# Performance work log

Hardware: AMD Instinct MI355X
Metric: run time of the kernel (lower is better)

## Reference

```python
import jax, jax.numpy as jnp
import numpy as np

N_TOPICS = 256
BATCH = 131072


def setup_inputs() -> dict:
    key = jax.random.key(0)
    k = jax.random.split(key, 6)
    n, b = N_TOPICS, BATCH
    s = 1.0 / np.sqrt(n)  # matches torch RNNCell uniform(-1/sqrt(h), 1/sqrt(h)) scale
    return {
        "z": jax.random.normal(k[0], (b, n), jnp.float32),
        "h0": jax.random.uniform(k[1], (1, n), jnp.float32),
        "W_ih": jax.random.uniform(k[2], (n, n), jnp.float32, -s, s),
        "W_hh": jax.random.uniform(k[3], (n, n), jnp.float32, -s, s),
        "b_ih": jax.random.uniform(k[4], (n,), jnp.float32, -s, s),
        "b_hh": jax.random.uniform(k[5], (n,), jnp.float32, -s, s),
    }


def _stick_breaking(x):
    # torch.distributions.StickBreakingTransform._call
    D = x.shape[-1]
    offset = jnp.arange(D, 0, -1, dtype=x.dtype)          # [D, D-1, ..., 1]
    zc = jax.nn.sigmoid(x - jnp.log(offset))
    fi = jnp.finfo(x.dtype)
    zc = jnp.clip(zc, fi.tiny, 1.0 - fi.eps)              # _clipped_sigmoid
    z_cumprod = jnp.cumprod(1.0 - zc, axis=-1)
    ones = jnp.ones(x.shape[:-1] + (1,), x.dtype)
    return jnp.concatenate([zc, ones], -1) * jnp.concatenate([ones, z_cumprod], -1)


def reference(z, h0, W_ih, W_hh, b_ih, b_hh):
    n = W_ih.shape[0]
    D = n - 1
    b = b_ih + b_hh
    # step 0: rnncell(h0) with zero hidden state -> tanh(h0 @ W_ih.T + b_ih + b_hh)
    h1 = jnp.tanh(h0 @ W_ih.T + b)                        # (1, n)
    # steps i>0: rnncell(h, h) = tanh(h @ (W_ih + W_hh).T + b_ih + b_hh)
    Wc = (W_ih + W_hh).T

    def step(h, _):
        hn = jnp.tanh(h @ Wc + b)
        return hn, hn

    _, hs = jax.lax.scan(step, h1, None, length=D - 1)    # (D-1, 1, n)
    H = jnp.concatenate([h1[None], hs], axis=0)[:, 0, :]  # (D, n)
    eta = jax.nn.sigmoid(H @ z.T).T                       # (batch, D)
    return _stick_breaking(eta)                           # (batch, n)
```

## Files before the change

### kernel.cpp

```cpp
#include <hip/hip_runtime.h>

#define NTOP 256

typedef __attribute__((ext_vector_type(8))) short bf16x8;
typedef __attribute__((ext_vector_type(4))) float f32x4;

__device__ inline unsigned int packbf(float x) {
  unsigned int u = __float_as_uint(x);
  unsigned int r = (u + 0x7fffu + ((u >> 16) & 1u)) & 0xffff0000u;
  float res = x - __uint_as_float(r);
  unsigned int u2 = __float_as_uint(res);
  unsigned int r2 = u2 + 0x7fffu + ((u2 >> 16) & 1u);
  return r | (r2 >> 16);
}

__device__ inline float tanh_fast(float x) {
  float e = __expf(2.f * x);
  return 1.f - 2.f / (e + 1.f);
}

__global__ __launch_bounds__(1024) void rsbc_recur(
    const float* __restrict__ Wih, const float* __restrict__ Whh,
    const float* __restrict__ bih, const float* __restrict__ bhh,
    const float* __restrict__ h0, unsigned int* __restrict__ Hpack) {
  __shared__ float hA[4][68], hB[4][68];
  const int tid = threadIdx.x;
  const int j = tid >> 2, qt = tid & 3, k0 = qt * 64;
  const float bj = bih[j] + bhh[j];

  float4 w[16];
  const float4* wp = reinterpret_cast<const float4*>(Wih + j * NTOP + k0);
#pragma unroll
  for (int q = 0; q < 16; ++q) w[q] = wp[q];

  if (tid < NTOP) hA[tid >> 6][tid & 63] = h0[tid];
  __syncthreads();

  {
    const float* hq = hA[qt];
    float a0 = 0.f, a1 = 0.f, a2 = 0.f, a3 = 0.f;
#pragma unroll
    for (int q = 0; q < 16; ++q) {
      float4 hv = *reinterpret_cast<const float4*>(hq + 4 * q);
      a0 += hv.x * w[q].x; a1 += hv.y * w[q].y;
      a2 += hv.z * w[q].z; a3 += hv.w * w[q].w;
    }
    float s = (a0 + a1) + (a2 + a3);
    s += __shfl_xor(s, 1);
    s += __shfl_xor(s, 2);
    if (qt == 0) {
      float v = tanh_fast(s + bj);
      hB[j >> 6][j & 63] = v;
      Hpack[j] = packbf(v);
    }
  }
  const float4* wq = reinterpret_cast<const float4*>(Whh + j * NTOP + k0);
#pragma unroll
  for (int q = 0; q < 16; ++q) {
    float4 t = wq[q];
    w[q].x += t.x; w[q].y += t.y; w[q].z += t.z; w[q].w += t.w;
  }
  __syncthreads();

  for (int s = 1; s < 255; ++s) {
    const float(*hr)[68] = (s & 1) ? hB : hA;
    float(*hw)[68] = (s & 1) ? hA : hB;
    const float* hq = hr[qt];
    float a0 = 0.f, a1 = 0.f, a2 = 0.f, a3 = 0.f;
#pragma unroll
    for (int q = 0; q < 16; ++q) {
      float4 hv = *reinterpret_cast<const float4*>(hq + 4 * q);
      a0 += hv.x * w[q].x; a1 += hv.y * w[q].y;
      a2 += hv.z * w[q].z; a3 += hv.w * w[q].w;
    }
    float sv = (a0 + a1) + (a2 + a3);
    sv += __shfl_xor(sv, 1);
    sv += __shfl_xor(sv, 2);
    if (qt == 0) {
      float v = tanh_fast(sv + bj);
      hw[j >> 6][j & 63] = v;
      Hpack[s * NTOP + j] = packbf(v);
    }
    __syncthreads();
  }
}

__global__ __launch_bounds__(512, 2) void rsbc_gemm_sb(
    const float* __restrict__ z, const unsigned int* __restrict__ Hpack,
    float* __restrict__ out) {
  constexpr int AS = 72;
  constexpr int BS = 72;
  constexpr int ES = 260;
  __shared__ __align__(16) char smem[135168];
  __shared__ float logtab[256];
  ushort* Ahi = reinterpret_cast<ushort*>(smem);
  ushort* Alo = Ahi + 128 * AS;
  ushort* Bhi = Alo + 128 * AS;
  ushort* Blo = Bhi + 256 * BS;
  float* eta = reinterpret_cast<float*>(smem);
  float* segT = eta + 128 * ES;

  const int tid = threadIdx.x;
  const size_t row0 = (size_t)blockIdx.x * 128;
  const int wid = tid >> 6, lane = tid & 63;
  const int wr = wid >> 2, wc = wid & 3;
  const int l15 = lane & 15, l4 = lane >> 4;

  if (tid < 255) logtab[tid] = logf((float)(255 - tid));

  f32x4 acc[4][4];
#pragma unroll
  for (int mt = 0; mt < 4; ++mt)
#pragma unroll
    for (int nt = 0; nt < 4; ++nt) acc[mt][nt] = (f32x4){0.f, 0.f, 0.f, 0.f};

  for (int kc = 0; kc < 4; ++kc) {
    const int kb = kc * 64;
    float4 zreg[4];
#pragma unroll
    for (int it = 0; it < 4; ++it) {
      int idx = tid + 512 * it;
      int r = idx >> 4, q = idx & 15;
      zreg[it] = *reinterpret_cast<const float4*>(
          z + (row0 + r) * NTOP + kb + 4 * q);
    }
    uint4 hreg[8];
#pragma unroll
    for (int it = 0; it < 8; ++it) {
      int idx = tid + 512 * it;
      int r = idx >> 4, q = idx & 15;
      hreg[it] = (r < 255)
                     ? *reinterpret_cast<const uint4*>(
                           Hpack + r * NTOP + kb + 4 * q)
                     : make_uint4(0u, 0u, 0u, 0u);
    }
    __syncthreads();
#pragma unroll
    for (int it = 0; it < 4; ++it) {
      int idx = tid + 512 * it;
      int r = idx >> 4, q = idx & 15;
      float4 v = zreg[it];
      unsigned int p0 = packbf(v.x), p1 = packbf(v.y),
                   p2 = packbf(v.z), p3 = packbf(v.w);
      *reinterpret_cast<ushort4*>(&Ahi[r * AS + 4 * q]) = make_ushort4(
          (ushort)(p0 >> 16), (ushort)(p1 >> 16),
          (ushort)(p2 >> 16), (ushort)(p3 >> 16));
      *reinterpret_cast<ushort4*>(&Alo[r * AS + 4 * q]) = make_ushort4(
          (ushort)(p0 & 0xffff), (ushort)(p1 & 0xffff),
          (ushort)(p2 & 0xffff), (ushort)(p3 & 0xffff));
    }
#pragma unroll
    for (int it = 0; it < 8; ++it) {
      int idx = tid + 512 * it;
      int r = idx >> 4, q = idx & 15;
      uint4 hv = hreg[it];
      *reinterpret_cast<ushort4*>(&Bhi[r * BS + 4 * q]) = make_ushort4(
          (ushort)(hv.x >> 16), (ushort)(hv.y >> 16),
          (ushort)(hv.z >> 16), (ushort)(hv.w >> 16));
      *reinterpret_cast<ushort4*>(&Blo[r * BS + 4 * q]) = make_ushort4(
          (ushort)(hv.x & 0xffff), (ushort)(hv.y & 0xffff),
          (ushort)(hv.z & 0xffff), (ushort)(hv.w & 0xffff));
    }
    __syncthreads();
#pragma unroll
    for (int ks = 0; ks < 2; ++ks) {
      const int ko = ks * 32 + l4 * 8;
      bf16x8 afh[4], afl[4], bfh[4], bfl[4];
#pragma unroll
      for (int mt = 0; mt < 4; ++mt) {
        int r = 64 * wr + 16 * mt + l15;
        afh[mt] = *reinterpret_cast<const bf16x8*>(&Ahi[r * AS + ko]);
        afl[mt] = *reinterpret_cast<const bf16x8*>(&Alo[r * AS + ko]);
      }
#pragma unroll
      for (int nt = 0; nt < 4; ++nt) {
        int n = 64 * wc + 16 * nt + l15;
        bfh[nt] = *reinterpret_cast<const bf16x8*>(&Bhi[n * BS + ko]);
        bfl[nt] = *reinterpret_cast<const bf16x8*>(&Blo[n * BS + ko]);
      }
#pragma unroll
      for (int mt = 0; mt < 4; ++mt)
#pragma unroll
        for (int nt = 0; nt < 4; ++nt) {
          acc[mt][nt] = __builtin_amdgcn_mfma_f32_16x16x32_bf16(
              afh[mt], bfh[nt], acc[mt][nt], 0, 0, 0);
          acc[mt][nt] = __builtin_amdgcn_mfma_f32_16x16x32_bf16(
              afh[mt], bfl[nt], acc[mt][nt], 0, 0, 0);
          acc[mt][nt] = __builtin_amdgcn_mfma_f32_16x16x32_bf16(
              afl[mt], bfh[nt], acc[mt][nt], 0, 0, 0);
        }
    }
  }
  __syncthreads();

#pragma unroll
  for (int mt = 0; mt < 4; ++mt) {
    int rbase = 64 * wr + 16 * mt + 4 * l4;
#pragma unroll
    for (int nt = 0; nt < 4; ++nt) {
      int c = 64 * wc + 16 * nt + l15;
#pragma unroll
      for (int i = 0; i < 4; ++i) {
        float x = acc[mt][nt][i];
        eta[(rbase + i) * ES + c] = 1.f / (1.f + __expf(-x));
      }
    }
  }
  __syncthreads();

  const int r = tid >> 2, qk = tid & 3;
  const int kbeg = 64 * qk, kend = (qk == 3) ? 255 : 64 * qk + 64;
  float* er = &eta[r * ES];
  {
    float cp = 1.f;
#pragma unroll 4
    for (int k = kbeg; k < kend; ++k) {
      float x = er[k] - logtab[k];
      float zc = 1.f / (1.f + __expf(-x));
      zc = fminf(fmaxf(zc, 1.1754943508222875e-38f), 0.99999988079071045f);
      er[k] = zc * cp;
      cp *= 1.f - zc;
    }
    segT[r * 4 + qk] = cp;
  }
  __syncthreads();
  {
    float p = 1.f;
    if (qk > 0) p *= segT[r * 4 + 0];
    if (qk > 1) p *= segT[r * 4 + 1];
    if (qk > 2) p *= segT[r * 4 + 2];
    if (qk > 0) {
#pragma unroll 4
      for (int k = kbeg; k < kend; ++k) er[k] *= p;
    }
    if (qk == 3) er[255] = p * segT[r * 4 + 3];
  }
  __syncthreads();

#pragma unroll
  for (int it = 0; it < 16; ++it) {
    int idx = tid + 512 * it;
    int rr = idx >> 6, cq = idx & 63;
    float4 vv = *reinterpret_cast<const float4*>(&eta[rr * ES + 4 * cq]);
    *reinterpret_cast<float4*>(&out[(row0 + rr) * NTOP + 4 * cq]) = vv;
  }
}

extern "C" void kernel_launch(void* const* d_in, const int* in_sizes, int n_in,
                              void* d_out, int out_size, void* d_ws, size_t ws_size,
                              hipStream_t stream) {
  const float* z   = (const float*)d_in[0];
  const float* h0  = (const float*)d_in[1];
  const float* Wih = (const float*)d_in[2];
  const float* Whh = (const float*)d_in[3];
  const float* bih = (const float*)d_in[4];
  const float* bhh = (const float*)d_in[5];
  float* out = (float*)d_out;
  unsigned int* Hpack = (unsigned int*)d_ws;

  rsbc_recur<<<1, 1024, 0, stream>>>(Wih, Whh, bih, bhh, h0, Hpack);
  const int nrows = out_size / NTOP;
  const int blocks = nrows / 128;
  rsbc_gemm_sb<<<blocks, 512, 0, stream>>>(z, Hpack, out);
}
```

Measured before the change: 335.1 us.

## Rework recurrence partitioning and fuse stick-breaking scan into GEMM epilogue registers

The recurrence kernel now splits each dot product across waves, combining partial sums through shared memory with DPP reductions. The GEMM kernel moves to a smaller K-chunk with XOR-swizzled shared tiles, cutting LDS use to allow more blocks per CU. The stick-breaking cumulative product is now done as a log-space prefix scan in registers on the accumulators (DPP scan16 plus a cross-wave row total). This removes the eta shared-memory round trip and the serial per-row loop, and output is stored straight from registers. The log-space product (exp of summed softplus) can differ numerically from the direct cumprod, the explicit clip is gone, and the output stores are 4-byte strided rather than float4.

```diff
diff --git a/kernel.cpp b/kernel.cpp
--- a/kernel.cpp
+++ b/kernel.cpp
@@ -19,86 +19,94 @@
   return 1.f - 2.f / (e + 1.f);
 }
 
-__global__ __launch_bounds__(1024) void rsbc_recur(
+template <int CTRL>
+__device__ inline float dpp_f(float v) {
+  return __int_as_float(__builtin_amdgcn_update_dpp(
+      0, __float_as_int(v), CTRL, 0xf, 0xf, true));
+}
+
+__device__ inline float scan16(float v) {
+  float s = v;
+  s += dpp_f<0x111>(s);
+  s += dpp_f<0x112>(s);
+  s += dpp_f<0x114>(s);
+  s += dpp_f<0x118>(s);
+  return s;
+}
+
+__global__ __launch_bounds__(1024, 4) void rsbc_recur(
     const float* __restrict__ Wih, const float* __restrict__ Whh,
     const float* __restrict__ bih, const float* __restrict__ bhh,
     const float* __restrict__ h0, unsigned int* __restrict__ Hpack) {
-  __shared__ float hA[4][68], hB[4][68];
+  __shared__ __align__(16) float hsh[NTOP];
+  __shared__ __align__(16) float pw[16 * 260];
   const int tid = threadIdx.x;
-  const int j = tid >> 2, qt = tid & 3, k0 = qt * 64;
-  const float bj = bih[j] + bhh[j];
-
-  float4 w[16];
-  const float4* wp = reinterpret_cast<const float4*>(Wih + j * NTOP + k0);
-#pragma unroll
-  for (int q = 0; q < 16; ++q) w[q] = wp[q];
-
-  if (tid < NTOP) hA[tid >> 6][tid & 63] = h0[tid];
+  const int w = tid >> 6, l = tid & 63;
+  const int jr = tid >> 2, p4 = tid & 3;
+  const float bj = bih[jr] + bhh[jr];
+
+  float4 L[16];
+#pragma unroll
+  for (int c = 0; c < 4; ++c)
+#pragma unroll
+    for (int g = 0; g < 4; ++g)
+      L[4 * c + g] = *reinterpret_cast<const float4*>(
+          Wih + (4 * l + c) * NTOP + 16 * w + 4 * g);
+
+  if (tid < NTOP) hsh[tid] = h0[tid];
   __syncthreads();
 
-  {
-    const float* hq = hA[qt];
-    float a0 = 0.f, a1 = 0.f, a2 = 0.f, a3 = 0.f;
-#pragma unroll
-    for (int q = 0; q < 16; ++q) {
-      float4 hv = *reinterpret_cast<const float4*>(hq + 4 * q);
-      a0 += hv.x * w[q].x; a1 += hv.y * w[q].y;
-      a2 += hv.z * w[q].z; a3 += hv.w * w[q].w;
-    }
-    float s = (a0 + a1) + (a2 + a3);
-    s += __shfl_xor(s, 1);
-    s += __shfl_xor(s, 2);
-    if (qt == 0) {
-      float v = tanh_fast(s + bj);
-      hB[j >> 6][j & 63] = v;
-      Hpack[j] = packbf(v);
+#pragma unroll 1
+  for (int s = 0; s < 255; ++s) {
+    float4 hv[4];
+#pragma unroll
+    for (int g = 0; g < 4; ++g)
+      hv[g] = *reinterpret_cast<const float4*>(hsh + 16 * w + 4 * g);
+    float a[4] = {0.f, 0.f, 0.f, 0.f};
+#pragma unroll
+    for (int c = 0; c < 4; ++c)
+#pragma unroll
+      for (int g = 0; g < 4; ++g) {
+        a[c] += hv[g].x * L[4 * c + g].x;
+        a[c] += hv[g].y * L[4 * c + g].y;
+        a[c] += hv[g].z * L[4 * c + g].z;
+        a[c] += hv[g].w * L[4 * c + g].w;
+      }
+    *reinterpret_cast<float4*>(&pw[w * 260 + 4 * l]) =
+        make_float4(a[0], a[1], a[2], a[3]);
+    __syncthreads();
+    float v = pw[(4 * p4 + 0) * 260 + jr] + pw[(4 * p4 + 1) * 260 + jr] +
+              pw[(4 * p4 + 2) * 260 + jr] + pw[(4 * p4 + 3) * 260 + jr];
+    v += dpp_f<0xB1>(v);
+    v += dpp_f<0x4E>(v);
+    if (p4 == 0) {
+      float hn = tanh_fast(v + bj);
+      hsh[jr] = hn;
+      Hpack[s * NTOP + jr] = packbf(hn);
+    }
+    __syncthreads();
+    if (s == 0) {
+#pragma unroll
+      for (int c = 0; c < 4; ++c)
+#pragma unroll
+        for (int g = 0; g < 4; ++g) {
+          float4 t = *reinterpret_cast<const float4*>(
+              Whh + (4 * l + c) * NTOP + 16 * w + 4 * g);
+          L[4 * c + g].x += t.x; L[4 * c + g].y += t.y;
+          L[4 * c + g].z += t.z; L[4 * c + g].w += t.w;
+        }
     }
   }
-  const float4* wq = reinterpret_cast<const float4*>(Whh + j * NTOP + k0);
-#pragma unroll
-  for (int q = 0; q < 16; ++q) {
-    float4 t = wq[q];
-    w[q].x += t.x; w[q].y += t.y; w[q].z += t.z; w[q].w += t.w;
-  }
-  __syncthreads();
-
-  for (int s = 1; s < 255; ++s) {
-    const float(*hr)[68] = (s & 1) ? hB : hA;
-    float(*hw)[68] = (s & 1) ? hA : hB;
-    const float* hq = hr[qt];
-    float a0 = 0.f, a1 = 0.f, a2 = 0.f, a3 = 0.f;
-#pragma unroll
-    for (int q = 0; q < 16; ++q) {
-      float4 hv = *reinterpret_cast<const float4*>(hq + 4 * q);
-      a0 += hv.x * w[q].x; a1 += hv.y * w[q].y;
-      a2 += hv.z * w[q].z; a3 += hv.w * w[q].w;
-    }
-    float sv = (a0 + a1) + (a2 + a3);
-    sv += __shfl_xor(sv, 1);
-    sv += __shfl_xor(sv, 2);
-    if (qt == 0) {
-      float v = tanh_fast(sv + bj);
-      hw[j >> 6][j & 63] = v;
-      Hpack[s * NTOP + j] = packbf(v);
-    }
-    __syncthreads();
-  }
-}
-
-__global__ __launch_bounds__(512, 2) void rsbc_gemm_sb(
+}
+
+__global__ __launch_bounds__(512, 4) void rsbc_gemm_sb(
     const float* __restrict__ z, const unsigned int* __restrict__ Hpack,
     float* __restrict__ out) {
-  constexpr int AS = 72;
-  constexpr int BS = 72;
-  constexpr int ES = 260;
-  __shared__ __align__(16) char smem[135168];
-  __shared__ float logtab[256];
-  ushort* Ahi = reinterpret_cast<ushort*>(smem);
-  ushort* Alo = Ahi + 128 * AS;
-  ushort* Bhi = Alo + 128 * AS;
-  ushort* Blo = Bhi + 256 * BS;
-  float* eta = reinterpret_cast<float*>(smem);
-  float* segT = eta + 128 * ES;
+  __shared__ __align__(16) char smem[49152];
+  __shared__ float logtab[NTOP];
+  __shared__ float rowT[128 * 5];
+  char* Ab = smem;
+  char* Bb = smem + 16384;
 
   const int tid = threadIdx.x;
   const size_t row0 = (size_t)blockIdx.x * 128;
@@ -106,7 +114,7 @@
   const int wr = wid >> 2, wc = wid & 3;
   const int l15 = lane & 15, l4 = lane >> 4;
 
-  if (tid < 255) logtab[tid] = logf((float)(255 - tid));
+  if (tid < NTOP) logtab[tid] = (tid < 255) ? __logf((float)(255 - tid)) : 0.f;
 
   f32x4 acc[4][4];
 #pragma unroll
@@ -114,136 +122,130 @@
 #pragma unroll
     for (int nt = 0; nt < 4; ++nt) acc[mt][nt] = (f32x4){0.f, 0.f, 0.f, 0.f};
 
-  for (int kc = 0; kc < 4; ++kc) {
-    const int kb = kc * 64;
-    float4 zreg[4];
-#pragma unroll
-    for (int it = 0; it < 4; ++it) {
-      int idx = tid + 512 * it;
-      int r = idx >> 4, q = idx & 15;
+  for (int kc = 0; kc < 8; ++kc) {
+    const int kb = kc * 32;
+    float4 zreg[2];
+#pragma unroll
+    for (int it = 0; it < 2; ++it) {
+      int idx = tid + 512 * it;
+      int r = idx >> 3, q = idx & 7;
       zreg[it] = *reinterpret_cast<const float4*>(
           z + (row0 + r) * NTOP + kb + 4 * q);
     }
-    uint4 hreg[8];
-#pragma unroll
-    for (int it = 0; it < 8; ++it) {
-      int idx = tid + 512 * it;
-      int r = idx >> 4, q = idx & 15;
-      hreg[it] = (r < 255)
-                     ? *reinterpret_cast<const uint4*>(
-                           Hpack + r * NTOP + kb + 4 * q)
-                     : make_uint4(0u, 0u, 0u, 0u);
-    }
-    __syncthreads();
+    uint4 hreg[4];
 #pragma unroll
     for (int it = 0; it < 4; ++it) {
       int idx = tid + 512 * it;
-      int r = idx >> 4, q = idx & 15;
+      int r = idx >> 3, q = idx & 7;
+      hreg[it] = (r < 255) ? *reinterpret_cast<const uint4*>(
+                                 Hpack + r * NTOP + kb + 4 * q)
+                           : make_uint4(0u, 0u, 0u, 0u);
+    }
+    __syncthreads();
+#pragma unroll
+    for (int it = 0; it < 2; ++it) {
+      int idx = tid + 512 * it;
+      int r = idx >> 3, q = idx & 7;
+      int sw = (r & 7) << 4;
       float4 v = zreg[it];
       unsigned int p0 = packbf(v.x), p1 = packbf(v.y),
                    p2 = packbf(v.z), p3 = packbf(v.w);
-      *reinterpret_cast<ushort4*>(&Ahi[r * AS + 4 * q]) = make_ushort4(
-          (ushort)(p0 >> 16), (ushort)(p1 >> 16),
-          (ushort)(p2 >> 16), (ushort)(p3 >> 16));
-      *reinterpret_cast<ushort4*>(&Alo[r * AS + 4 * q]) = make_ushort4(
-          (ushort)(p0 & 0xffff), (ushort)(p1 & 0xffff),
-          (ushort)(p2 & 0xffff), (ushort)(p3 & 0xffff));
-    }
-#pragma unroll
-    for (int it = 0; it < 8; ++it) {
-      int idx = tid + 512 * it;
-      int r = idx >> 4, q = idx & 15;
-      uint4 hv = hreg[it];
-      *reinterpret_cast<ushort4*>(&Bhi[r * BS + 4 * q]) = make_ushort4(
-          (ushort)(hv.x >> 16), (ushort)(hv.y >> 16),
-          (ushort)(hv.z >> 16), (ushort)(hv.w >> 16));
-      *reinterpret_cast<ushort4*>(&Blo[r * BS + 4 * q]) = make_ushort4(
-          (ushort)(hv.x & 0xffff), (ushort)(hv.y & 0xffff),
-          (ushort)(hv.z & 0xffff), (ushort)(hv.w & 0xffff));
-    }
-    __syncthreads();
-#pragma unroll
-    for (int ks = 0; ks < 2; ++ks) {
-      const int ko = ks * 32 + l4 * 8;
-      bf16x8 afh[4], afl[4], bfh[4], bfl[4];
+      *reinterpret_cast<ushort4*>(Ab + r * 128 + ((8 * q) ^ sw)) =
+          make_ushort4((ushort)(p0 >> 16), (ushort)(p1 >> 16),
+                       (ushort)(p2 >> 16), (ushort)(p3 >> 16));
+      *reinterpret_cast<ushort4*>(Ab + r * 128 + ((64 + 8 * q) ^ sw)) =
+          make_ushort4((ushort)(p0 & 0xffff), (ushort)(p1 & 0xffff),
+                       (ushort)(p2 & 0xffff), (ushort)(p3 & 0xffff));
+    }
+#pragma unroll
+    for (int it = 0; it < 4; ++it) {
+      int idx = tid + 512 * it;
+      int r = idx >> 3, q = idx & 7;
+      int sw = (r & 7) << 4;
+      uint4 h = hreg[it];
+      *reinterpret_cast<ushort4*>(Bb + r * 128 + ((8 * q) ^ sw)) =
+          make_ushort4((ushort)(h.x >> 16), (ushort)(h.y >> 16),
+                       (ushort)(h.z >> 16), (ushort)(h.w >> 16));
+      *reinterpret_cast<ushort4*>(Bb + r * 128 + ((64 + 8 * q) ^ sw)) =
+          make_ushort4((ushort)(h.x & 0xffff), (ushort)(h.y & 0xffff),
+                       (ushort)(h.z & 0xffff), (ushort)(h.w & 0xffff));
+    }
+    __syncthreads();
+    bf16x8 ah[4], al[4];
+#pragma unroll
+    for (int mt = 0; mt < 4; ++mt) {
+      int r = 64 * wr + 16 * mt + l15;
+      int sw = (r & 7) << 4;
+      ah[mt] = *reinterpret_cast<const bf16x8*>(Ab + r * 128 + ((16 * l4) ^ sw));
+      al[mt] = *reinterpret_cast<const bf16x8*>(
+          Ab + r * 128 + ((64 + 16 * l4) ^ sw));
+    }
+#pragma unroll
+    for (int nt = 0; nt < 4; ++nt) {
+      int n = 64 * wc + 16 * nt + l15;
+      int sw = (n & 7) << 4;
+      bf16x8 bh = *reinterpret_cast<const bf16x8*>(
+          Bb + n * 128 + ((16 * l4) ^ sw));
+      bf16x8 bl = *reinterpret_cast<const bf16x8*>(
+          Bb + n * 128 + ((64 + 16 * l4) ^ sw));
 #pragma unroll
       for (int mt = 0; mt < 4; ++mt) {
-        int r = 64 * wr + 16 * mt + l15;
-        afh[mt] = *reinterpret_cast<const bf16x8*>(&Ahi[r * AS + ko]);
-        afl[mt] = *reinterpret_cast<const bf16x8*>(&Alo[r * AS + ko]);
-      }
+        acc[mt][nt] = __builtin_amdgcn_mfma_f32_16x16x32_bf16(
+            ah[mt], bh, acc[mt][nt], 0, 0, 0);
+        acc[mt][nt] = __builtin_amdgcn_mfma_f32_16x16x32_bf16(
+            ah[mt], bl, acc[mt][nt], 0, 0, 0);
+        acc[mt][nt] = __builtin_amdgcn_mfma_f32_16x16x32_bf16(
+            al[mt], bh, acc[mt][nt], 0, 0, 0);
+      }
+    }
+  }
+
+  float lt[4];
+#pragma unroll
+  for (int nt = 0; nt < 4; ++nt) lt[nt] = logtab[64 * wc + 16 * nt + l15];
+#pragma unroll
+  for (int mt = 0; mt < 4; ++mt)
+#pragma unroll
+    for (int i = 0; i < 4; ++i) {
+      float carry = 0.f;
 #pragma unroll
       for (int nt = 0; nt < 4; ++nt) {
-        int n = 64 * wc + 16 * nt + l15;
-        bfh[nt] = *reinterpret_cast<const bf16x8*>(&Bhi[n * BS + ko]);
-        bfl[nt] = *reinterpret_cast<const bf16x8*>(&Blo[n * BS + ko]);
-      }
-#pragma unroll
-      for (int mt = 0; mt < 4; ++mt)
-#pragma unroll
-        for (int nt = 0; nt < 4; ++nt) {
-          acc[mt][nt] = __builtin_amdgcn_mfma_f32_16x16x32_bf16(
-              afh[mt], bfh[nt], acc[mt][nt], 0, 0, 0);
-          acc[mt][nt] = __builtin_amdgcn_mfma_f32_16x16x32_bf16(
-              afh[mt], bfl[nt], acc[mt][nt], 0, 0, 0);
-          acc[mt][nt] = __builtin_amdgcn_mfma_f32_16x16x32_bf16(
-              afl[mt], bfh[nt], acc[mt][nt], 0, 0, 0);
+        float a = acc[mt][nt][i];
+        float t1 = __expf(-a);
+        float s1 = __builtin_amdgcn_rcpf(1.f + t1);
+        float x = s1 - lt[nt];
+        float t = __expf(-x);
+        float zc = __builtin_amdgcn_rcpf(1.f + t);
+        float sp = x + __logf(1.f + t);
+        if ((wc == 3) && (nt == 3) && (l15 == 15)) {
+          zc = 1.f; sp = 0.f;
         }
-    }
-  }
+        float incl = scan16(sp);
+        float Sl = carry + (incl - sp);
+        acc[mt][nt][i] = zc * __expf(-Sl);
+        carry += __shfl(incl, 15, 16);
+      }
+      if (l15 == 0)
+        rowT[(64 * wr + 16 * mt + 4 * l4 + i) * 5 + wc] = carry;
+    }
   __syncthreads();
 
 #pragma unroll
-  for (int mt = 0; mt < 4; ++mt) {
-    int rbase = 64 * wr + 16 * mt + 4 * l4;
-#pragma unroll
-    for (int nt = 0; nt < 4; ++nt) {
-      int c = 64 * wc + 16 * nt + l15;
-#pragma unroll
-      for (int i = 0; i < 4; ++i) {
-        float x = acc[mt][nt][i];
-        eta[(rbase + i) * ES + c] = 1.f / (1.f + __expf(-x));
-      }
-    }
-  }
-  __syncthreads();
-
-  const int r = tid >> 2, qk = tid & 3;
-  const int kbeg = 64 * qk, kend = (qk == 3) ? 255 : 64 * qk + 64;
-  float* er = &eta[r * ES];
-  {
-    float cp = 1.f;
-#pragma unroll 4
-    for (int k = kbeg; k < kend; ++k) {
-      float x = er[k] - logtab[k];
-      float zc = 1.f / (1.f + __expf(-x));
-      zc = fminf(fmaxf(zc, 1.1754943508222875e-38f), 0.99999988079071045f);
-      er[k] = zc * cp;
-      cp *= 1.f - zc;
-    }
-    segT[r * 4 + qk] = cp;
-  }
-  __syncthreads();
-  {
-    float p = 1.f;
-    if (qk > 0) p *= segT[r * 4 + 0];
-    if (qk > 1) p *= segT[r * 4 + 1];
-    if (qk > 2) p *= segT[r * 4 + 2];
-    if (qk > 0) {
-#pragma unroll 4
-      for (int k = kbeg; k < kend; ++k) er[k] *= p;
-    }
-    if (qk == 3) er[255] = p * segT[r * 4 + 3];
-  }
-  __syncthreads();
-
-#pragma unroll
-  for (int it = 0; it < 16; ++it) {
-    int idx = tid + 512 * it;
-    int rr = idx >> 6, cq = idx & 63;
-    float4 vv = *reinterpret_cast<const float4*>(&eta[rr * ES + 4 * cq]);
-    *reinterpret_cast<float4*>(&out[(row0 + rr) * NTOP + 4 * cq]) = vv;
-  }
+  for (int mt = 0; mt < 4; ++mt)
+#pragma unroll
+    for (int i = 0; i < 4; ++i) {
+      int r = 64 * wr + 16 * mt + 4 * l4 + i;
+      float ew = 1.f;
+      if (wc > 0) {
+        float W = rowT[r * 5 + 0];
+        if (wc > 1) W += rowT[r * 5 + 1];
+        if (wc > 2) W += rowT[r * 5 + 2];
+        ew = __expf(-W);
+      }
+      float* op = out + (row0 + r) * NTOP + 64 * wc + l15;
+#pragma unroll
+      for (int nt = 0; nt < 4; ++nt) op[16 * nt] = acc[mt][nt][i] * ew;
+    }
 }
 
 extern "C" void kernel_launch(void* const* d_in, const int* in_sizes, int n_in,
```

Result: slower. 478.2 us (+42.7%).
